# Kernel tuning notes

Hardware: AMD Instinct MI355X
Metric: run time of the kernel (lower is better)

## Reference

```python
import jax, jax.numpy as jnp
import numpy as np

N = 50000        # nodes
E = 800000       # edges
R = 8            # relations
G = 64           # g_dim
H1 = 64          # h1_dim
H2 = 32          # h2_dim (per-head for transformer, output for sage)
HEADS = 4
EPS = 1e-5       # BatchNorm eps


def setup_inputs() -> dict:
    key = jax.random.key(0)
    ks = jax.random.split(key, 16)
    def rn(k, shape, scale=0.05):
        return jax.random.normal(k, shape, dtype=jnp.float32) * scale
    return {
        "node_features": jax.random.normal(ks[0], (N, G), dtype=jnp.float32),
        "node_type": jax.random.randint(ks[1], (N,), 0, 3),
        "edge_index": jax.random.randint(ks[2], (2, E), 0, N),
        "edge_type": jax.random.randint(ks[3], (E,), 0, R),
        # RGCNConv params (per-relation weight + root weight + bias)
        "rgcn_w": rn(ks[4], (R, G, H1)),
        "rgcn_root": rn(ks[5], (G, H1)),
        "rgcn_bias": jnp.zeros((H1,), jnp.float32),
        "bn1_g": jnp.ones((H1,), jnp.float32),
        "bn1_b": jnp.zeros((H1,), jnp.float32),
        # TransformerConv params (q/k/v projections + skip)
        "wq": rn(ks[6], (H1, HEADS * H2)), "bq": jnp.zeros((HEADS * H2,), jnp.float32),
        "wk": rn(ks[7], (H1, HEADS * H2)), "bk": jnp.zeros((HEADS * H2,), jnp.float32),
        "wv": rn(ks[8], (H1, HEADS * H2)), "bv": jnp.zeros((HEADS * H2,), jnp.float32),
        "wskip": rn(ks[9], (H1, HEADS * H2)), "bskip": jnp.zeros((HEADS * H2,), jnp.float32),
        "bn2_g": jnp.ones((HEADS * H2,), jnp.float32),
        "bn2_b": jnp.zeros((HEADS * H2,), jnp.float32),
        # SAGEConv params (lin_l on aggregated neighbors has bias; lin_r on root has none)
        "sage_wl": rn(ks[10], (HEADS * H2, H2)), "sage_bl": jnp.zeros((H2,), jnp.float32),
        "sage_wr": rn(ks[11], (HEADS * H2, H2)),
        "bn3_g": jnp.ones((H2,), jnp.float32),
        "bn3_b": jnp.zeros((H2,), jnp.float32),
    }


def _bn(x, g, b):
    # BatchNorm1d in training mode: biased batch statistics over nodes
    m = x.mean(0)
    v = x.var(0)
    return g * (x - m) * jax.lax.rsqrt(v + EPS) + b


def _match(res, d):
    # F.pad(res, (0, d - c)): pads with zeros if d > c, truncates if d < c
    c = res.shape[1]
    if d > c:
        return jnp.pad(res, ((0, 0), (0, d - c)))
    return res[:, :d]


def _forward(node_features, rgcn_w, rgcn_root, rgcn_bias, bn1_g, bn1_b,
             wq, bq, wk, bk, wv, bv, wskip, bskip, bn2_g, bn2_b,
             sage_wl, sage_bl, sage_wr, bn3_g, bn3_b,
             edge_index, edge_type):
    src, dst = edge_index[0], edge_index[1]
    x = node_features
    residual = x

    # ---- RGCNConv: per-relation transform, per-relation mean aggregation, sum over relations ----
    xr = jnp.einsum('nf,rfh->nrh', x, rgcn_w)            # [N,R,H1]
    msg = xr[src, edge_type]                              # [E,H1]
    seg = dst * R + edge_type                             # segment per (node, relation)
    sums = jax.ops.segment_sum(msg, seg, num_segments=N * R)
    cnt = jax.ops.segment_sum(jnp.ones((E,), msg.dtype), seg, num_segments=N * R)
    agg = (sums / jnp.maximum(cnt, 1.0)[:, None]).reshape(N, R, H1).sum(1)
    h = agg + x @ rgcn_root + rgcn_bias
    h = jax.nn.leaky_relu(_bn(h, bn1_g, bn1_b))
    x = h + _match(residual, h.shape[1])
    residual = x

    # ---- TransformerConv: edge softmax attention, concat heads, + skip projection ----
    q = (x @ wq + bq).reshape(N, HEADS, H2)
    k = (x @ wk + bk).reshape(N, HEADS, H2)
    v = (x @ wv + bv).reshape(N, HEADS, H2)
    logits = (q[dst] * k[src]).sum(-1) / jnp.sqrt(jnp.float32(H2))  # [E,HEADS]
    mx = jax.ops.segment_max(logits, dst, num_segments=N)
    ex = jnp.exp(logits - mx[dst])
    den = jax.ops.segment_sum(ex, dst, num_segments=N)
    alpha = ex / jnp.maximum(den[dst], 1e-16)
    out = jax.ops.segment_sum(alpha[:, :, None] * v[src], dst, num_segments=N)
    h = out.reshape(N, HEADS * H2) + x @ wskip + bskip
    h = jax.nn.leaky_relu(_bn(h, bn2_g, bn2_b))
    x = h + _match(residual, h.shape[1])
    residual = x

    # ---- SAGEConv: mean neighbor aggregation + root transform ----
    nsum = jax.ops.segment_sum(x[src], dst, num_segments=N)
    ncnt = jax.ops.segment_sum(jnp.ones((E,), x.dtype), dst, num_segments=N)
    nmean = nsum / jnp.maximum(ncnt, 1.0)[:, None]
    h = nmean @ sage_wl + sage_bl + x @ sage_wr
    h = jax.nn.leaky_relu(_bn(h, bn3_g, bn3_b))
    return h + _match(residual, h.shape[1])


def reference(node_features, node_type, edge_index, edge_type,
              rgcn_w, rgcn_root, rgcn_bias, bn1_g, bn1_b,
              wq, bq, wk, bk, wv, bv, wskip, bskip, bn2_g, bn2_b,
              sage_wl, sage_bl, sage_wr, bn3_g, bn3_b):
    # node_type is unused by the original forward
    return _forward(node_features, rgcn_w, rgcn_root, rgcn_bias, bn1_g, bn1_b,
                    wq, bq, wk, bk, wv, bv, wskip, bskip, bn2_g, bn2_b,
                    sage_wl, sage_bl, sage_wr, bn3_g, bn3_b,
                    edge_index, edge_type)
```

## Files before the change

kernel.cpp:

```cpp
#include <hip/hip_runtime.h>
#include <stdint.h>

#define NN 50000
#define NE 800000
#define NR (NN*8)
#define SCAN_BS 512
#define NB2 782
#define INV_N (1.0f/50000.0f)
#define BN_EPS 1e-5f

typedef unsigned short ushort_t;
typedef unsigned char uchar_t;
typedef short bf16x8 __attribute__((ext_vector_type(8)));
typedef float f32x4 __attribute__((ext_vector_type(4)));
typedef float f32x2 __attribute__((ext_vector_type(2)));

__device__ __forceinline__ ushort_t f2bf(float f){
    unsigned int u = __float_as_uint(f);
    u += 0x7FFFu + ((u >> 16) & 1u);
    return (ushort_t)(u >> 16);
}
__device__ __forceinline__ float bf2f(ushort_t h){ return __uint_as_float(((unsigned int)h) << 16); }
__device__ __forceinline__ float bflo(unsigned int u){ return __uint_as_float(u << 16); }
__device__ __forceinline__ float bfhi(unsigned int u){ return __uint_as_float(u & 0xFFFF0000u); }

__device__ __forceinline__ unsigned int f4_to_fp8(float a, float b, float c, float d){
    int v = __builtin_amdgcn_cvt_pk_fp8_f32(a, b, 0, false);
    v = __builtin_amdgcn_cvt_pk_fp8_f32(c, d, v, true);
    return (unsigned int)v;
}
__device__ __forceinline__ void fp8_to_f4(unsigned int u, float& a, float& b, float& c, float& d){
    f32x2 lo = __builtin_amdgcn_cvt_pk_f32_fp8(u, false);
    f32x2 hi = __builtin_amdgcn_cvt_pk_f32_fp8(u, true);
    a = lo.x; b = lo.y; c = hi.x; d = hi.y;
}

__global__ void k_deg(const int* __restrict__ ei, const int* __restrict__ et,
                      int* __restrict__ deg, uint2* __restrict__ sr){
    int e = blockIdx.x*256 + threadIdx.x;
    if (e < NE){
        int seg = ei[NE + e]*8 + et[e];
        int rank = atomicAdd(&deg[seg], 1);
        uint2 o; o.x = (unsigned)seg; o.y = (unsigned)rank;
        sr[e] = o;
    }
}

__global__ void k_scan1(const int* __restrict__ deg, int* __restrict__ tmp, int* __restrict__ bsum){
    __shared__ int s[SCAN_BS];
    int t = threadIdx.x;
    int i = blockIdx.x*SCAN_BS + t;
    s[t] = (i < NR) ? deg[i] : 0;
    __syncthreads();
    for (int off = 1; off < SCAN_BS; off <<= 1){
        int add = (t >= off) ? s[t-off] : 0;
        __syncthreads();
        s[t] += add;
        __syncthreads();
    }
    if (i < NR) tmp[i] = s[t];
    if (t == SCAN_BS-1) bsum[blockIdx.x] = s[t];
}

__global__ void k_scan2(int* __restrict__ bsum){
    __shared__ int s[NB2];
    int t = threadIdx.x;
    if (t < NB2) s[t] = bsum[t];
    __syncthreads();
    if (t == 0){
        int acc = 0;
        for (int i = 0; i < NB2; ++i){ acc += s[i]; s[i] = acc; }
    }
    __syncthreads();
    if (t < NB2) bsum[t] = s[t];
}

__global__ void k_scan3(const int* __restrict__ tmp, const int* __restrict__ bsum, int* __restrict__ rs){
    int i = blockIdx.x*256 + threadIdx.x;
    if (i < NR){
        int b = i >> 9;
        int off = (b > 0) ? bsum[b-1] : 0;
        rs[i+1] = tmp[i] + off;
        if (i == 0) rs[0] = 0;
    }
}

__global__ void k_fill(const int* __restrict__ ei, const uint2* __restrict__ sr,
                       const int* __restrict__ rs, int* __restrict__ csr){
    int e = blockIdx.x*256 + threadIdx.x;
    if (e < NE){
        uint2 s = sr[e];
        csr[rs[s.x] + (int)s.y] = ei[e];
    }
}

__global__ void k_prep(const float* __restrict__ nf,
                       const float* __restrict__ rgcn_w, const float* __restrict__ root,
                       const float* __restrict__ wq, const float* __restrict__ wk,
                       const float* __restrict__ wv, const float* __restrict__ wsk,
                       const float* __restrict__ bq, const float* __restrict__ bk,
                       const float* __restrict__ bv, const float* __restrict__ bsk,
                       const float* __restrict__ wl, const float* __restrict__ wr,
                       ushort_t* __restrict__ xb, uchar_t* __restrict__ xb8,
                       ushort_t* __restrict__ Wcat,
                       ushort_t* __restrict__ Wt2, float* __restrict__ bcat,
                       ushort_t* __restrict__ Wsage){
    int i = blockIdx.x*256 + threadIdx.x;
    const int NXB = NN*16;
    if (i < NXB){
        float4 v = ((const float4*)nf)[i];
        ushort4 h;
        h.x = f2bf(v.x); h.y = f2bf(v.y); h.z = f2bf(v.z); h.w = f2bf(v.w);
        ((ushort4*)xb)[i] = h;
        ((unsigned int*)xb8)[i] = f4_to_fp8(v.x, v.y, v.z, v.w);
        return;
    }
    int j = i - NXB;
    if (j < 64*576){
        int h = j / 576, k = j - h*576;
        float v = (k < 512) ? rgcn_w[(size_t)k*64 + h] : root[(size_t)(k-512)*64 + h];
        Wcat[j] = f2bf(v);
    } else if (j < 64*576 + 512*64){
        int jj = j - 64*576;
        int c = jj >> 6, k = jj & 63;
        int mt = c >> 7, cc = c & 127;
        const float* W = (mt==0)?wq:(mt==1)?wk:(mt==2)?wv:wsk;
        Wt2[jj] = f2bf(W[(size_t)k*128 + cc]);
    } else if (j < 64*576 + 512*64 + 512){
        int c = j - (64*576 + 512*64);
        int mt = c >> 7, cc = c & 127;
        const float* B = (mt==0)?bq:(mt==1)?bk:(mt==2)?bv:bsk;
        bcat[c] = B[cc];
    } else if (j < 64*576 + 512*64 + 512 + 32*256){
        int jj = j - (64*576 + 512*64 + 512);
        int c = jj >> 8, k = jj & 255;
        float v = (k < 128) ? wr[(size_t)k*32 + c] : wl[(size_t)(k-128)*32 + c];
        Wsage[jj] = f2bf(v);
    }
}

__global__ __launch_bounds__(256) void rgcn_fused(const ushort_t* __restrict__ xb,
                                                  const uchar_t* __restrict__ xb8,
                                                  const int* __restrict__ rs,
                                                  const int* __restrict__ csr,
                                                  const ushort_t* __restrict__ Wcat,
                                                  const float* __restrict__ bias,
                                                  float* __restrict__ h1pre){
    __shared__ ushort_t Ml[16*520];
    int w = threadIdx.x >> 6, lane = threadIdx.x & 63;
    int quad = lane >> 4, l4 = lane & 15;
    int row0 = blockIdx.x * 16;
    int n0 = row0 + w*4;
    int rsel = (lane < 9 ? lane : 8);
    int rb = rs[n0*8 + rsel];
    int eb0 = __shfl(rb, 0);
    int dg0 = __shfl(rb, 8) - eb0;
    int idx = (lane < dg0) ? csr[eb0 + lane] : 0;
    for (int j = 0; j < 4; ++j){
        int lrow = (w*4 + j)*520;
        int ebase = __shfl(rb, 0);
        int enext = __shfl(rb, 8);
        int rb_next = 0, idxn = 0;
        if (j < 3){
            rb_next = rs[(n0 + j + 1)*8 + rsel];
            idxn = csr[min(enext + lane, NE - 1)];
        }
        int e0a = __shfl(rb, quad),     e1a = __shfl(rb, quad + 1);
        int e0b = __shfl(rb, quad + 4), e1b = __shfl(rb, quad + 5);
        int oa = e0a - ebase, la = e1a - e0a;
        int ob = e0b - ebase, lb = e1b - e0b;
        int ml = max(la, lb);
        ml = max(ml, __shfl_xor(ml, 16));
        ml = max(ml, __shfl_xor(ml, 32));
        float aa0=0.f, aa1=0.f, aa2=0.f, aa3=0.f;
        float ab0=0.f, ab1=0.f, ab2=0.f, ab3=0.f;
        for (int i = 0; i < ml; i += 4){
            int sA[4], sB[4];
            bool vA[4], vB[4];
#pragma unroll
            for (int u = 0; u < 4; ++u){
                int jA = oa + i + u, jB = ob + i + u;
                vA[u] = (i + u) < la;
                vB[u] = (i + u) < lb;
                int tA = __shfl(idx, jA & 63);
                int tB = __shfl(idx, jB & 63);
                if (jA >= 64 && vA[u]) tA = csr[ebase + jA];
                if (jB >= 64 && vB[u]) tB = csr[ebase + jB];
                sA[u] = vA[u] ? tA : 0;
                sB[u] = vB[u] ? tB : 0;
            }
            unsigned int uA[4], uB[4];
#pragma unroll
            for (int u = 0; u < 4; ++u){
                uA[u] = *(const unsigned int*)(xb8 + (size_t)sA[u]*64 + l4*4);
                uB[u] = *(const unsigned int*)(xb8 + (size_t)sB[u]*64 + l4*4);
            }
#pragma unroll
            for (int u = 0; u < 4; ++u){
                float f0,f1,f2,f3;
                fp8_to_f4(uA[u],f0,f1,f2,f3);
                if (vA[u]){ aa0+=f0; aa1+=f1; aa2+=f2; aa3+=f3; }
                fp8_to_f4(uB[u],f0,f1,f2,f3);
                if (vB[u]){ ab0+=f0; ab1+=f1; ab2+=f2; ab3+=f3; }
            }
        }
        float inva = 1.f / fmaxf((float)la, 1.f);
        float invb = 1.f / fmaxf((float)lb, 1.f);
        ushort4 oA, oB;
        oA.x = f2bf(aa0*inva); oA.y = f2bf(aa1*inva); oA.z = f2bf(aa2*inva); oA.w = f2bf(aa3*inva);
        oB.x = f2bf(ab0*invb); oB.y = f2bf(ab1*invb); oB.z = f2bf(ab2*invb); oB.w = f2bf(ab3*invb);
        *(ushort4*)&Ml[lrow + quad*64 + l4*4] = oA;
        *(ushort4*)&Ml[lrow + (quad + 4)*64 + l4*4] = oB;
        if (j < 3){
            rb = rb_next;
            int ebn = __shfl(rb, 0);
            int dgn = __shfl(rb, 8) - ebn;
            idx = (lane < dgn) ? idxn : 0;
        }
    }
    __syncthreads();
    int m = l4;
    f32x4 acc = {};
#pragma unroll
    for (int kt = 0; kt < 18; ++kt){
        int kk = kt*32 + quad*8;
        bf16x8 a;
        if (kt < 16) a = *(const bf16x8*)&Ml[m*520 + kk];
        else         a = *(const bf16x8*)(xb + (size_t)(row0 + m)*64 + (kk - 512));
        bf16x8 b = *(const bf16x8*)(Wcat + (size_t)(w*16 + m)*576 + kk);
        acc = __builtin_amdgcn_mfma_f32_16x16x32_bf16(a, b, acc, 0, 0, 0);
    }
    int col = w*16 + m;
    float bz = bias[col];
#pragma unroll
    for (int i = 0; i < 4; ++i){
        int rr = row0 + quad*4 + i;
        h1pre[(size_t)rr*64 + col] = acc[i] + bz;
    }
}

__global__ void bn1_finalize(const float* __restrict__ sums, const float* __restrict__ sumsq,
                             const float* __restrict__ g1, const float* __restrict__ b1,
                             float* __restrict__ A1, float* __restrict__ C1){
    int c = threadIdx.x;
    if (c < 64){
        float m = sums[c] * INV_N;
        float v = sumsq[c] * INV_N - m*m;
        float rsv = rsqrtf(fmaxf(v, 0.f) + BN_EPS);
        float A = rsv * g1[c];
        A1[c] = A;
        C1[c] = b1[c] - m * A;
    }
}

#define QS 132
#define BS 68
__global__ __launch_bounds__(256) void gemm_qkvs(const float* __restrict__ h1pre,
                                                 const float* __restrict__ nf,
                                                 const float* __restrict__ A1, const float* __restrict__ C1,
                                                 const ushort_t* __restrict__ Wt2,
                                                 const float* __restrict__ bcat,
                                                 ushort_t* __restrict__ qb,
                                                 uchar_t* __restrict__ kb8,
                                                 ushort_t* __restrict__ vb,
                                                 ushort_t* __restrict__ sb){
    __shared__ ushort_t Bs[256*BS];
    __shared__ ushort_t pl[4][16*QS];
    int w = threadIdx.x >> 6, lane = threadIdx.x & 63;
    int m = lane & 15, quad = lane >> 4;
    int r0 = blockIdx.x*64 + w*16;
    int cg = blockIdx.y;
    int row = r0 + m;
    {
        int t = threadIdx.x;
        const ushort_t* wsrc = Wt2 + (size_t)cg*256*64;
#pragma unroll
        for (int u0 = 0; u0 < 8; ++u0){
            int u = u0*256 + t;
            int r = u >> 3, c8 = (u & 7)*8;
            *(uint4*)&Bs[r*BS + c8] = *(const uint4*)(wsrc + u*8);
        }
    }
    bf16x8 afrag[2];
#pragma unroll
    for (int kt = 0; kt < 2; ++kt){
        int db = kt*32 + quad*8;
        bf16x8 f = (bf16x8){0,0,0,0,0,0,0,0};
        if (row < NN){
            float4 h0 = *(const float4*)(h1pre + (size_t)row*64 + db);
            float4 h1 = *(const float4*)(h1pre + (size_t)row*64 + db + 4);
            float4 n0 = *(const float4*)(nf + (size_t)row*64 + db);
            float4 n1 = *(const float4*)(nf + (size_t)row*64 + db + 4);
            float4 a0 = *(const float4*)(A1 + db);
            float4 a1 = *(const float4*)(A1 + db + 4);
            float4 c0 = *(const float4*)(C1 + db);
            float4 c1 = *(const float4*)(C1 + db + 4);
            float hh[8] = {h0.x,h0.y,h0.z,h0.w,h1.x,h1.y,h1.z,h1.w};
            float nn[8] = {n0.x,n0.y,n0.z,n0.w,n1.x,n1.y,n1.z,n1.w};
            float AA[8] = {a0.x,a0.y,a0.z,a0.w,a1.x,a1.y,a1.z,a1.w};
            float CC[8] = {c0.x,c0.y,c0.z,c0.w,c1.x,c1.y,c1.z,c1.w};
#pragma unroll
            for (int e = 0; e < 8; ++e){
                float y = fmaf(hh[e], AA[e], CC[e]);
                y = (y >= 0.f) ? y : 0.01f*y;
                f[e] = (short)f2bf(y + nn[e]);
            }
        }
        afrag[kt] = f;
    }
    __syncthreads();
    f32x4 acc[16] = {};
#pragma unroll
    for (int kt = 0; kt < 2; ++kt){
        int kk = kt*32 + quad*8;
#pragma unroll
        for (int ct = 0; ct < 16; ++ct){
            bf16x8 b = *(const bf16x8*)&Bs[(size_t)(ct*16 + m)*BS + kk];
            acc[ct] = __builtin_amdgcn_mfma_f32_16x16x32_bf16(afrag[kt], b, acc[ct], 0, 0, 0);
        }
    }
#pragma unroll
    for (int ct = 0; ct < 8; ++ct){
        int g = cg*256 + ct*16 + m;
        float bz = bcat[g];
        int cc = g & 127;
#pragma unroll
        for (int i = 0; i < 4; ++i)
            pl[w][(quad*4 + i)*QS + cc] = f2bf(acc[ct][i] + bz);
    }
    if (cg == 0){
#pragma unroll
        for (int t = 0; t < 4; ++t){
            int u = t*64 + lane;
            int r = u >> 4, c = (u & 15)*8;
            int gr = r0 + r;
            if (gr < NN) *(uint4*)(qb + (size_t)gr*128 + c) = *(const uint4*)&pl[w][r*QS + c];
        }
    } else {
#pragma unroll
        for (int t = 0; t < 4; ++t){
            int u = t*64 + lane;
            int r = u >> 4, c = (u & 15)*8;
            int gr = r0 + r;
            if (gr < NN) *(uint4*)(vb + (size_t)gr*128 + c) = *(const uint4*)&pl[w][r*QS + c];
        }
    }
#pragma unroll
    for (int ct = 8; ct < 16; ++ct){
        int g = cg*256 + ct*16 + m;
        float bz = bcat[g];
        int cc = g & 127;
#pragma unroll
        for (int i = 0; i < 4; ++i)
            pl[w][(quad*4 + i)*QS + cc] = f2bf(acc[ct][i] + bz);
    }
    if (cg == 0){
#pragma unroll
        for (int t = 0; t < 4; ++t){
            int u = t*64 + lane;
            int r = u >> 4, c = (u & 15)*8;
            int gr = r0 + r;
            if (gr < NN){
                uint4 kk4 = *(const uint4*)&pl[w][r*QS + c];
                uint2 o;
                o.x = f4_to_fp8(bflo(kk4.x), bfhi(kk4.x), bflo(kk4.y), bfhi(kk4.y));
                o.y = f4_to_fp8(bflo(kk4.z), bfhi(kk4.z), bflo(kk4.w), bfhi(kk4.w));
                *(uint2*)(kb8 + (size_t)gr*128 + c) = o;
            }
        }
    } else {
#pragma unroll
        for (int t = 0; t < 4; ++t){
            int u = t*64 + lane;
            int r = u >> 4, c = (u & 15)*8;
            int gr = r0 + r;
            if (gr < NN) *(uint4*)(sb + (size_t)gr*128 + c) = *(const uint4*)&pl[w][r*QS + c];
        }
    }
}

__global__ __launch_bounds__(256) void sage_gemm(const ushort_t* __restrict__ x2b,
                                                 const ushort_t* __restrict__ nmeanb,
                                                 const ushort_t* __restrict__ Wsage,
                                                 const float* __restrict__ bl,
                                                 float* __restrict__ h3){
    int wv = threadIdx.x >> 6, lane = threadIdx.x & 63;
    int r0 = blockIdx.x*64 + wv*16;
    int m = lane & 15, quad = lane >> 4;
    int row = r0 + m;
    f32x4 acc[2] = {};
#pragma unroll
    for (int kt = 0; kt < 8; ++kt){
        int kk = kt*32 + quad*8;
        bf16x8 a;
        if (row < NN){
            const ushort_t* ap = (kt < 4) ? (x2b + (size_t)row*128 + kk)
                                          : (nmeanb + (size_t)row*128 + (kk - 128));
            a = *(const bf16x8*)ap;
        } else {
            a = (bf16x8){0,0,0,0,0,0,0,0};
        }
#pragma unroll
        for (int ct = 0; ct < 2; ++ct){
            bf16x8 b = *(const bf16x8*)(Wsage + (size_t)(ct*16 + m)*256 + kk);
            acc[ct] = __builtin_amdgcn_mfma_f32_16x16x32_bf16(a, b, acc[ct], 0, 0, 0);
        }
    }
#pragma unroll
    for (int ct = 0; ct < 2; ++ct){
        int col = ct*16 + m;
        float bz = bl[col];
#pragma unroll
        for (int i = 0; i < 4; ++i){
            int rr = r0 + quad*4 + i;
            if (rr < NN) h3[(size_t)rr*32 + col] = acc[ct][i] + bz;
        }
    }
}

template<int C>
__global__ __launch_bounds__(256) void bn_stats(const float* __restrict__ X, int ld,
                                                float* __restrict__ sums, float* __restrict__ sumsq){
    __shared__ float s1[256], s2[256];
    int t = threadIdx.x;
    int c = t & (C-1);
    const int rpb = 256 / C;
    int r = blockIdx.x * rpb + (t / C);
    int rstride = gridDim.x * rpb;
    float a = 0.f, b = 0.f;
    for (; r < NN; r += rstride){
        float v = X[(size_t)r*ld + c];
        a += v; b += v*v;
    }
    s1[t] = a; s2[t] = b;
    __syncthreads();
    for (int off = 128; off >= C; off >>= 1){
        if (t < off){ s1[t] += s1[t+off]; s2[t] += s2[t+off]; }
        __syncthreads();
    }
    if (t < C){ atomicAdd(&sums[t], s1[t]); atomicAdd(&sumsq[t], s2[t]); }
}

__device__ __forceinline__ float bn_leaky(float z, float m, float rsv, float g, float b){
    float y = (z - m) * rsv * g + b;
    return y >= 0.f ? y : 0.01f * y;
}

__global__ void bn_apply2(const float* __restrict__ h2, const float* __restrict__ h1pre,
                          const float* __restrict__ nf,
                          const float* __restrict__ g1, const float* __restrict__ b1,
                          const float* __restrict__ s1, const float* __restrict__ q1,
                          const float* __restrict__ g2, const float* __restrict__ b2,
                          const float* __restrict__ s2, const float* __restrict__ q2,
                          float* __restrict__ x2r, ushort_t* __restrict__ x2b,
                          uchar_t* __restrict__ x28){
    int i = blockIdx.x*256 + threadIdx.x;
    if (i >= NN*128) return;
    int n = i >> 7, c = i & 127;
    float m2 = s2[c] * INV_N;
    float v2 = q2[c] * INV_N - m2*m2;
    float rsv2 = rsqrtf(fmaxf(v2, 0.f) + BN_EPS);
    float val = bn_leaky(h2[i], m2, rsv2, g2[c], b2[c]);
    if (c < 64){
        float m1 = s1[c] * INV_N;
        float v1 = q1[c] * INV_N - m1*m1;
        float rsv1 = rsqrtf(fmaxf(v1, 0.f) + BN_EPS);
        val += bn_leaky(h1pre[(size_t)n*64 + c], m1, rsv1, g1[c], b1[c]) + nf[(size_t)n*64 + c];
    }
    if (c < 32) x2r[(size_t)n*32 + c] = val;
    x2b[i] = f2bf(val);
    int p = __builtin_amdgcn_cvt_pk_fp8_f32(val, val, 0, false);
    x28[i] = (uchar_t)(p & 0xFF);
}

__global__ void bn_apply3(const float* __restrict__ h3, const float* __restrict__ x2r,
                          const float* __restrict__ g, const float* __restrict__ b,
                          const float* __restrict__ sums, const float* __restrict__ sumsq,
                          float* __restrict__ out){
    int i = blockIdx.x*256 + threadIdx.x;
    if (i >= NN*32) return;
    int c = i & 31;
    float m = sums[c] * INV_N;
    float v = sumsq[c] * INV_N - m*m;
    float rsv = rsqrtf(fmaxf(v, 0.f) + BN_EPS);
    out[i] = bn_leaky(h3[i], m, rsv, g[c], b[c]) + x2r[i];
}

__global__ __launch_bounds__(256) void attn_kernel(const ushort_t* __restrict__ qb,
                                                   const uchar_t* __restrict__ kb8,
                                                   const ushort_t* __restrict__ vb,
                                                   const ushort_t* __restrict__ sb,
                                                   const int* __restrict__ rs,
                                                   const int* __restrict__ csr,
                                                   float* __restrict__ h2){
    int w = threadIdx.x >> 6, lane = threadIdx.x & 63;
    int n = blockIdx.x*4 + w;
    if (n >= NN) return;
    int half = lane >> 5, l5 = lane & 31;
    int e0 = rs[n*8], e1 = rs[n*8 + 8];
    int deg = e1 - e0;
    uint2 qu = *(const uint2*)(qb + (size_t)n*128 + l5*4);
    uint2 sbv = *(const uint2*)(sb + (size_t)n*128 + l5*4);
    float q0 = bflo(qu.x), q1 = bfhi(qu.x), q2 = bflo(qu.y), q3 = bfhi(qu.y);
    const float scale = 0.17677669529663687f;
    int idx = 0;
    if (lane < deg) idx = csr[e0 + lane];
    int dcap = min(deg, 64);
    int nt = (dcap + 7) >> 3;
    float den = 0.f, a0 = 0.f, a1 = 0.f, a2 = 0.f, a3 = 0.f;
    for (int t = 0; t < nt; ++t){
        int i2 = t*8 + half*4;
        int j0 = i2, j1 = i2+1, j2 = i2+2, j3 = i2+3;
        bool v0 = j0 < dcap, v1 = j1 < dcap, v2 = j2 < dcap, v3 = j3 < dcap;
        int s0 = __shfl(idx, j0 & 63); s0 = v0 ? s0 : 0;
        int s1 = __shfl(idx, j1 & 63); s1 = v1 ? s1 : 0;
        int s2 = __shfl(idx, j2 & 63); s2 = v2 ? s2 : 0;
        int s3 = __shfl(idx, j3 & 63); s3 = v3 ? s3 : 0;
        unsigned int ku0 = *(const unsigned int*)(kb8 + (size_t)s0*128 + l5*4);
        unsigned int ku1 = *(const unsigned int*)(kb8 + (size_t)s1*128 + l5*4);
        unsigned int ku2 = *(const unsigned int*)(kb8 + (size_t)s2*128 + l5*4);
        unsigned int ku3 = *(const unsigned int*)(kb8 + (size_t)s3*128 + l5*4);
        uint2 vv0 = *(const uint2*)(vb + (size_t)s0*128 + l5*4);
        uint2 vv1 = *(const uint2*)(vb + (size_t)s1*128 + l5*4);
        uint2 vv2 = *(const uint2*)(vb + (size_t)s2*128 + l5*4);
        uint2 vv3 = *(const uint2*)(vb + (size_t)s3*128 + l5*4);
        float ka, kb_, kc, kd;
        fp8_to_f4(ku0, ka, kb_, kc, kd);
        float p0 = q0*ka + q1*kb_ + q2*kc + q3*kd;
        fp8_to_f4(ku1, ka, kb_, kc, kd);
        float p1 = q0*ka + q1*kb_ + q2*kc + q3*kd;
        fp8_to_f4(ku2, ka, kb_, kc, kd);
        float p2 = q0*ka + q1*kb_ + q2*kc + q3*kd;
        fp8_to_f4(ku3, ka, kb_, kc, kd);
        float p3 = q0*ka + q1*kb_ + q2*kc + q3*kd;
        p0 += __shfl_xor(p0, 1); p1 += __shfl_xor(p1, 1); p2 += __shfl_xor(p2, 1); p3 += __shfl_xor(p3, 1);
        p0 += __shfl_xor(p0, 2); p1 += __shfl_xor(p1, 2); p2 += __shfl_xor(p2, 2); p3 += __shfl_xor(p3, 2);
        p0 += __shfl_xor(p0, 4); p1 += __shfl_xor(p1, 4); p2 += __shfl_xor(p2, 4); p3 += __shfl_xor(p3, 4);
        float w0 = v0 ? __expf(p0 * scale) : 0.f;
        float w1 = v1 ? __expf(p1 * scale) : 0.f;
        float w2 = v2 ? __expf(p2 * scale) : 0.f;
        float w3 = v3 ? __expf(p3 * scale) : 0.f;
        den += w0 + w1 + w2 + w3;
        a0 += w0*bflo(vv0.x) + w1*bflo(vv1.x) + w2*bflo(vv2.x) + w3*bflo(vv3.x);
        a1 += w0*bfhi(vv0.x) + w1*bfhi(vv1.x) + w2*bfhi(vv2.x) + w3*bfhi(vv3.x);
        a2 += w0*bflo(vv0.y) + w1*bflo(vv1.y) + w2*bflo(vv2.y) + w3*bflo(vv3.y);
        a3 += w0*bfhi(vv0.y) + w1*bfhi(vv1.y) + w2*bfhi(vv2.y) + w3*bfhi(vv3.y);
    }
    for (int e = 64 + half; e < deg; e += 2){
        int s = csr[e0 + e];
        unsigned int ku = *(const unsigned int*)(kb8 + (size_t)s*128 + l5*4);
        uint2 vv = *(const uint2*)(vb + (size_t)s*128 + l5*4);
        float ka, kb_, kc, kd;
        fp8_to_f4(ku, ka, kb_, kc, kd);
        float p = q0*ka + q1*kb_ + q2*kc + q3*kd;
        p += __shfl_xor(p, 1);
        p += __shfl_xor(p, 2);
        p += __shfl_xor(p, 4);
        float wg = __expf(p * scale);
        den += wg;
        a0 += wg*bflo(vv.x); a1 += wg*bfhi(vv.x);
        a2 += wg*bflo(vv.y); a3 += wg*bfhi(vv.y);
    }
    den += __shfl_xor(den, 32);
    a0 += __shfl_xor(a0, 32); a1 += __shfl_xor(a1, 32);
    a2 += __shfl_xor(a2, 32); a3 += __shfl_xor(a3, 32);
    if (half == 0){
        float inv = (den > 0.f) ? 1.f/den : 0.f;
        float4 o;
        o.x = bflo(sbv.x) + a0*inv;
        o.y = bfhi(sbv.x) + a1*inv;
        o.z = bflo(sbv.y) + a2*inv;
        o.w = bfhi(sbv.y) + a3*inv;
        *(float4*)(h2 + (size_t)n*128 + l5*4) = o;
    }
}

__global__ __launch_bounds__(256) void sage_agg(const uchar_t* __restrict__ x28,
                                                const int* __restrict__ rs,
                                                const int* __restrict__ csr,
                                                ushort_t* __restrict__ nmeanb){
    int w = threadIdx.x >> 6, lane = threadIdx.x & 63;
    int n = blockIdx.x*4 + w;
    if (n >= NN) return;
    int half = lane >> 5, l5 = lane & 31;
    int e0 = rs[n*8], e1 = rs[n*8 + 8];
    int deg = e1 - e0;
    int idx = 0;
    if (lane < deg) idx = csr[e0 + lane];
    int dcap = min(deg, 64);
    int nt = (dcap + 7) >> 3;
    float a0 = 0.f, a1 = 0.f, a2 = 0.f, a3 = 0.f;
    for (int t = 0; t < nt; ++t){
        int i2 = t*8 + half*4;
        int j0 = i2, j1 = i2+1, j2 = i2+2, j3 = i2+3;
        bool v0 = j0 < dcap, v1 = j1 < dcap, v2 = j2 < dcap, v3 = j3 < dcap;
        int s0 = __shfl(idx, j0 & 63); s0 = v0 ? s0 : 0;
        int s1 = __shfl(idx, j1 & 63); s1 = v1 ? s1 : 0;
        int s2 = __shfl(idx, j2 & 63); s2 = v2 ? s2 : 0;
        int s3 = __shfl(idx, j3 & 63); s3 = v3 ? s3 : 0;
        unsigned int u0 = *(const unsigned int*)(x28 + (size_t)s0*128 + l5*4);
        unsigned int u1 = *(const unsigned int*)(x28 + (size_t)s1*128 + l5*4);
        unsigned int u2 = *(const unsigned int*)(x28 + (size_t)s2*128 + l5*4);
        unsigned int u3 = *(const unsigned int*)(x28 + (size_t)s3*128 + l5*4);
        float fa, fb, fc, fd;
        if (v0){ fp8_to_f4(u0, fa, fb, fc, fd); a0 += fa; a1 += fb; a2 += fc; a3 += fd; }
        if (v1){ fp8_to_f4(u1, fa, fb, fc, fd); a0 += fa; a1 += fb; a2 += fc; a3 += fd; }
        if (v2){ fp8_to_f4(u2, fa, fb, fc, fd); a0 += fa; a1 += fb; a2 += fc; a3 += fd; }
        if (v3){ fp8_to_f4(u3, fa, fb, fc, fd); a0 += fa; a1 += fb; a2 += fc; a3 += fd; }
    }
    for (int e = 64 + half; e < deg; e += 2){
        int s = csr[e0 + e];
        unsigned int u = *(const unsigned int*)(x28 + (size_t)s*128 + l5*4);
        float fa, fb, fc, fd;
        fp8_to_f4(u, fa, fb, fc, fd);
        a0 += fa; a1 += fb; a2 += fc; a3 += fd;
    }
    a0 += __shfl_xor(a0, 32); a1 += __shfl_xor(a1, 32);
    a2 += __shfl_xor(a2, 32); a3 += __shfl_xor(a3, 32);
    if (half == 0){
        float inv = 1.f / fmaxf((float)deg, 1.f);
        ushort4 o;
        o.x = f2bf(a0*inv); o.y = f2bf(a1*inv); o.z = f2bf(a2*inv); o.w = f2bf(a3*inv);
        *(ushort4*)(nmeanb + (size_t)n*128 + l5*4) = o;
    }
}

extern "C" void kernel_launch(void* const* d_in, const int* in_sizes, int n_in,
                              void* d_out, int out_size, void* d_ws, size_t ws_size,
                              hipStream_t stream){
    const float* nf      = (const float*)d_in[0];
    const int*   ei      = (const int*)d_in[2];
    const int*   et      = (const int*)d_in[3];
    const float* rgcn_w  = (const float*)d_in[4];
    const float* root    = (const float*)d_in[5];
    const float* rbias   = (const float*)d_in[6];
    const float* bn1g    = (const float*)d_in[7];
    const float* bn1b    = (const float*)d_in[8];
    const float* wq      = (const float*)d_in[9];
    const float* bq      = (const float*)d_in[10];
    const float* wk      = (const float*)d_in[11];
    const float* bk      = (const float*)d_in[12];
    const float* wv      = (const float*)d_in[13];
    const float* bv      = (const float*)d_in[14];
    const float* wsk     = (const float*)d_in[15];
    const float* bsk     = (const float*)d_in[16];
    const float* bn2g    = (const float*)d_in[17];
    const float* bn2b    = (const float*)d_in[18];
    const float* wl      = (const float*)d_in[19];
    const float* bl      = (const float*)d_in[20];
    const float* wr      = (const float*)d_in[21];
    const float* bn3g    = (const float*)d_in[22];
    const float* bn3b    = (const float*)d_in[23];
    float* out = (float*)d_out;

    char* base = (char*)d_ws;
    size_t off = 0;
    auto take = [&](size_t bytes) -> char* {
        char* p = base + off;
        off += (bytes + 255) & ~(size_t)255;
        return p;
    };
    int*      deg    = (int*)take((size_t)NR*4);
    float*    bns    = (float*)take(1024*4);
    char*     zend   = base + off;
    int*      rs     = (int*)take((size_t)(NR+1)*4);
    int*      tmp    = (int*)take((size_t)NR*4);
    int*      bsum   = (int*)take(1024*4);
    uint2*    sr     = (uint2*)take((size_t)NE*8);
    int*      csr    = (int*)take((size_t)NE*4);
    ushort_t* Wcat   = (ushort_t*)take(64*576*2);
    ushort_t* Wt2    = (ushort_t*)take(512*64*2);
    float*    bcat   = (float*)take(512*4);
    ushort_t* Wsage  = (ushort_t*)take(32*256*2);
    ushort_t* xb     = (ushort_t*)take((size_t)NN*64*2);
    uchar_t*  xb8    = (uchar_t*)take((size_t)NN*64);
    float*    h1pre  = (float*)take((size_t)NN*64*4);
    float*    h2     = (float*)take((size_t)NN*128*4);
    float*    x2r    = (float*)take((size_t)NN*32*4);
    ushort_t* sb     = (ushort_t*)take((size_t)NN*128*2);
    char*     bigA   = take((size_t)NN*512*2);
    if (off > ws_size) return;

    ushort_t* qb     = (ushort_t*)(bigA + (size_t)NN*128);
    ushort_t* vb     = (ushort_t*)(bigA + (size_t)NN*384);
    uchar_t*  kb8    = (uchar_t*)(bigA + (size_t)NN*640);
    ushort_t* x2b    = (ushort_t*)bigA;
    uchar_t*  x28    = (uchar_t*)(bigA + (size_t)NN*256);
    ushort_t* nmeanb = (ushort_t*)(bigA + (size_t)NN*512);
    float*    h3     = (float*)(bigA + (size_t)NN*768);

    hipMemsetAsync(deg, 0, (size_t)(zend - (char*)deg), stream);

    const int PREP_N = NN*16 + 64*576 + 512*64 + 512 + 32*256;
    k_prep <<<(PREP_N+255)/256, 256, 0, stream>>>(nf, rgcn_w, root, wq, wk, wv, wsk,
                                                  bq, bk, bv, bsk, wl, wr,
                                                  xb, xb8, Wcat, Wt2, bcat, Wsage);
    k_deg  <<<(NE+255)/256, 256, 0, stream>>>(ei, et, deg, sr);
    k_scan1<<<NB2, SCAN_BS, 0, stream>>>(deg, tmp, bsum);
    k_scan2<<<1, 1024, 0, stream>>>(bsum);
    k_scan3<<<(NR+255)/256, 256, 0, stream>>>(tmp, bsum, rs);
    k_fill <<<(NE+255)/256, 256, 0, stream>>>(ei, sr, rs, csr);

    const int NB4 = (NN + 3) / 4;
    const int NBG = (NN + 63) / 64;

    rgcn_fused<<<NN/16, 256, 0, stream>>>(xb, xb8, rs, csr, Wcat, rbias, h1pre);
    bn_stats<64><<<256, 256, 0, stream>>>(h1pre, 64, bns + 0, bns + 64);
    bn1_finalize<<<1, 64, 0, stream>>>(bns + 0, bns + 64, bn1g, bn1b, bns + 448, bns + 512);

    gemm_qkvs<<<dim3(NBG, 2), 256, 0, stream>>>(h1pre, nf, bns + 448, bns + 512,
                                                Wt2, bcat, qb, kb8, vb, sb);
    attn_kernel<<<NB4, 256, 0, stream>>>(qb, kb8, vb, sb, rs, csr, h2);
    bn_stats<128><<<256, 256, 0, stream>>>(h2, 128, bns + 128, bns + 256);
    bn_apply2<<<(NN*128+255)/256, 256, 0, stream>>>(h2, h1pre, nf,
                                                    bn1g, bn1b, bns + 0, bns + 64,
                                                    bn2g, bn2b, bns + 128, bns + 256,
                                                    x2r, x2b, x28);

    sage_agg<<<NB4, 256, 0, stream>>>(x28, rs, csr, nmeanb);
    sage_gemm<<<NBG, 256, 0, stream>>>(x2b, nmeanb, Wsage, bl, h3);
    bn_stats<32><<<256, 256, 0, stream>>>(h3, 32, bns + 384, bns + 416);
    bn_apply3<<<(NN*32+255)/256, 256, 0, stream>>>(h3, x2r, bn3g, bn3b, bns + 384, bns + 416, out);
}
```

Measured before the change: 410.5 us.

## Aggregate RGCN per node with LDS atomics and store V as fp8

The CSR now stores each neighbour's relation in the low 3 bits of the source index, and a per-edge weight of 1/degree is precomputed at fill time. The RGCN kernel walks each node's full edge list once and accumulates weighted neighbour features into fp32 shared memory with atomic adds, replacing the per-relation segmented walk. Separately, the V projection is stored as fp8 instead of bf16, halving the bytes the attention kernel gathers per edge. The cost is shared-memory atomics, an extra weight array read, and lower precision in V.

```diff
diff --git a/kernel.cpp b/kernel.cpp
--- a/kernel.cpp
+++ b/kernel.cpp
@@ -8,6 +8,7 @@
 #define NB2 782
 #define INV_N (1.0f/50000.0f)
 #define BN_EPS 1e-5f
+#define ROWF 532
 
 typedef unsigned short ushort_t;
 typedef unsigned char uchar_t;
@@ -86,11 +87,16 @@
 }
 
 __global__ void k_fill(const int* __restrict__ ei, const uint2* __restrict__ sr,
-                       const int* __restrict__ rs, int* __restrict__ csr){
+                       const int* __restrict__ rs, int* __restrict__ csr,
+                       float* __restrict__ wgt){
     int e = blockIdx.x*256 + threadIdx.x;
     if (e < NE){
         uint2 s = sr[e];
-        csr[rs[s.x] + (int)s.y] = ei[e];
+        int b = rs[s.x];
+        int dgs = rs[s.x + 1] - b;
+        int pos = b + (int)s.y;
+        csr[pos] = ei[e]*8 + (int)(s.x & 7u);
+        wgt[pos] = 1.f / (float)dgs;
     }
 }
 
@@ -139,99 +145,93 @@
     }
 }
 
-__global__ __launch_bounds__(256) void rgcn_fused(const ushort_t* __restrict__ xb,
-                                                  const uchar_t* __restrict__ xb8,
-                                                  const int* __restrict__ rs,
-                                                  const int* __restrict__ csr,
-                                                  const ushort_t* __restrict__ Wcat,
-                                                  const float* __restrict__ bias,
-                                                  float* __restrict__ h1pre){
-    __shared__ ushort_t Ml[16*520];
+__global__ __launch_bounds__(256) void rgcn_fused2(const ushort_t* __restrict__ xb,
+                                                   const uchar_t* __restrict__ xb8,
+                                                   const int* __restrict__ rs,
+                                                   const int* __restrict__ csr,
+                                                   const float* __restrict__ wgt,
+                                                   const ushort_t* __restrict__ Wcat,
+                                                   const float* __restrict__ rbias,
+                                                   float* __restrict__ h1pre){
+    __shared__ float M[16*ROWF];
     int w = threadIdx.x >> 6, lane = threadIdx.x & 63;
-    int quad = lane >> 4, l4 = lane & 15;
+    int grp = lane >> 4, l4 = lane & 15;
     int row0 = blockIdx.x * 16;
-    int n0 = row0 + w*4;
-    int rsel = (lane < 9 ? lane : 8);
-    int rb = rs[n0*8 + rsel];
-    int eb0 = __shfl(rb, 0);
-    int dg0 = __shfl(rb, 8) - eb0;
-    int idx = (lane < dg0) ? csr[eb0 + lane] : 0;
+    {
+        float4 z = {0.f,0.f,0.f,0.f};
+        const int nf4 = 16*ROWF/4;
+        for (int i = threadIdx.x; i < nf4; i += 256) ((float4*)M)[i] = z;
+    }
+    __syncthreads();
     for (int j = 0; j < 4; ++j){
-        int lrow = (w*4 + j)*520;
-        int ebase = __shfl(rb, 0);
-        int enext = __shfl(rb, 8);
-        int rb_next = 0, idxn = 0;
-        if (j < 3){
-            rb_next = rs[(n0 + j + 1)*8 + rsel];
-            idxn = csr[min(enext + lane, NE - 1)];
-        }
-        int e0a = __shfl(rb, quad),     e1a = __shfl(rb, quad + 1);
-        int e0b = __shfl(rb, quad + 4), e1b = __shfl(rb, quad + 5);
-        int oa = e0a - ebase, la = e1a - e0a;
-        int ob = e0b - ebase, lb = e1b - e0b;
-        int ml = max(la, lb);
-        ml = max(ml, __shfl_xor(ml, 16));
-        ml = max(ml, __shfl_xor(ml, 32));
-        float aa0=0.f, aa1=0.f, aa2=0.f, aa3=0.f;
-        float ab0=0.f, ab1=0.f, ab2=0.f, ab3=0.f;
-        for (int i = 0; i < ml; i += 4){
-            int sA[4], sB[4];
-            bool vA[4], vB[4];
+        int n = row0 + w*4 + j;
+        int e0 = rs[n*8], e1 = rs[n*8 + 8];
+        int deg = e1 - e0;
+        int idx = 0; float wle = 0.f;
+        if (lane < deg){ idx = csr[e0 + lane]; wle = wgt[e0 + lane]; }
+        int dcap = min(deg, 64);
+        float* Mrow = M + (w*4 + j)*ROWF;
+        for (int t = 0; t < dcap; t += 16){
+            int sj[4]; float wj[4];
 #pragma unroll
             for (int u = 0; u < 4; ++u){
-                int jA = oa + i + u, jB = ob + i + u;
-                vA[u] = (i + u) < la;
-                vB[u] = (i + u) < lb;
-                int tA = __shfl(idx, jA & 63);
-                int tB = __shfl(idx, jB & 63);
-                if (jA >= 64 && vA[u]) tA = csr[ebase + jA];
-                if (jB >= 64 && vB[u]) tB = csr[ebase + jB];
-                sA[u] = vA[u] ? tA : 0;
-                sB[u] = vB[u] ? tB : 0;
+                int jj = t + grp*4 + u;
+                bool v = jj < dcap;
+                int s = __shfl(idx, jj & 63);
+                float ww = __shfl(wle, jj & 63);
+                sj[u] = v ? s : 0;
+                wj[u] = v ? ww : 0.f;
             }
-            unsigned int uA[4], uB[4];
-#pragma unroll
-            for (int u = 0; u < 4; ++u){
-                uA[u] = *(const unsigned int*)(xb8 + (size_t)sA[u]*64 + l4*4);
-                uB[u] = *(const unsigned int*)(xb8 + (size_t)sB[u]*64 + l4*4);
-            }
+            unsigned int ux[4];
+#pragma unroll
+            for (int u = 0; u < 4; ++u)
+                ux[u] = *(const unsigned int*)(xb8 + ((size_t)(unsigned)(sj[u] >> 3) << 6) + l4*4);
 #pragma unroll
             for (int u = 0; u < 4; ++u){
                 float f0,f1,f2,f3;
-                fp8_to_f4(uA[u],f0,f1,f2,f3);
-                if (vA[u]){ aa0+=f0; aa1+=f1; aa2+=f2; aa3+=f3; }
-                fp8_to_f4(uB[u],f0,f1,f2,f3);
-                if (vB[u]){ ab0+=f0; ab1+=f1; ab2+=f2; ab3+=f3; }
+                fp8_to_f4(ux[u], f0, f1, f2, f3);
+                float* p = Mrow + (sj[u] & 7)*64 + l4*4;
+                atomicAdd(p+0, wj[u]*f0);
+                atomicAdd(p+1, wj[u]*f1);
+                atomicAdd(p+2, wj[u]*f2);
+                atomicAdd(p+3, wj[u]*f3);
             }
         }
-        float inva = 1.f / fmaxf((float)la, 1.f);
-        float invb = 1.f / fmaxf((float)lb, 1.f);
-        ushort4 oA, oB;
-        oA.x = f2bf(aa0*inva); oA.y = f2bf(aa1*inva); oA.z = f2bf(aa2*inva); oA.w = f2bf(aa3*inva);
-        oB.x = f2bf(ab0*invb); oB.y = f2bf(ab1*invb); oB.z = f2bf(ab2*invb); oB.w = f2bf(ab3*invb);
-        *(ushort4*)&Ml[lrow + quad*64 + l4*4] = oA;
-        *(ushort4*)&Ml[lrow + (quad + 4)*64 + l4*4] = oB;
-        if (j < 3){
-            rb = rb_next;
-            int ebn = __shfl(rb, 0);
-            int dgn = __shfl(rb, 8) - ebn;
-            idx = (lane < dgn) ? idxn : 0;
+        for (int e = 64 + grp; e < deg; e += 4){
+            int s = csr[e0 + e];
+            float ww = wgt[e0 + e];
+            unsigned int ux = *(const unsigned int*)(xb8 + ((size_t)(unsigned)(s >> 3) << 6) + l4*4);
+            float f0,f1,f2,f3;
+            fp8_to_f4(ux, f0, f1, f2, f3);
+            float* p = Mrow + (s & 7)*64 + l4*4;
+            atomicAdd(p+0, ww*f0);
+            atomicAdd(p+1, ww*f1);
+            atomicAdd(p+2, ww*f2);
+            atomicAdd(p+3, ww*f3);
         }
     }
     __syncthreads();
-    int m = l4;
+    int m = l4, quad = grp;
     f32x4 acc = {};
 #pragma unroll
     for (int kt = 0; kt < 18; ++kt){
         int kk = kt*32 + quad*8;
         bf16x8 a;
-        if (kt < 16) a = *(const bf16x8*)&Ml[m*520 + kk];
-        else         a = *(const bf16x8*)(xb + (size_t)(row0 + m)*64 + (kk - 512));
+        if (kt < 16){
+            float4 v0 = *(const float4*)(M + m*ROWF + kk);
+            float4 v1 = *(const float4*)(M + m*ROWF + kk + 4);
+            a[0] = (short)f2bf(v0.x); a[1] = (short)f2bf(v0.y);
+            a[2] = (short)f2bf(v0.z); a[3] = (short)f2bf(v0.w);
+            a[4] = (short)f2bf(v1.x); a[5] = (short)f2bf(v1.y);
+            a[6] = (short)f2bf(v1.z); a[7] = (short)f2bf(v1.w);
+        } else {
+            a = *(const bf16x8*)(xb + (size_t)(row0 + m)*64 + (kk - 512));
+        }
         bf16x8 b = *(const bf16x8*)(Wcat + (size_t)(w*16 + m)*576 + kk);
         acc = __builtin_amdgcn_mfma_f32_16x16x32_bf16(a, b, acc, 0, 0, 0);
     }
     int col = w*16 + m;
-    float bz = bias[col];
+    float bz = rbias[col];
 #pragma unroll
     for (int i = 0; i < 4; ++i){
         int rr = row0 + quad*4 + i;
@@ -262,7 +262,7 @@
                                                  const float* __restrict__ bcat,
                                                  ushort_t* __restrict__ qb,
                                                  uchar_t* __restrict__ kb8,
-                                                 ushort_t* __restrict__ vb,
+                                                 uchar_t* __restrict__ vb8,
                                                  ushort_t* __restrict__ sb){
     __shared__ ushort_t Bs[256*BS];
     __shared__ ushort_t pl[4][16*QS];
@@ -342,7 +342,13 @@
             int u = t*64 + lane;
             int r = u >> 4, c = (u & 15)*8;
             int gr = r0 + r;
-            if (gr < NN) *(uint4*)(vb + (size_t)gr*128 + c) = *(const uint4*)&pl[w][r*QS + c];
+            if (gr < NN){
+                uint4 vv4 = *(const uint4*)&pl[w][r*QS + c];
+                uint2 o;
+                o.x = f4_to_fp8(bflo(vv4.x), bfhi(vv4.x), bflo(vv4.y), bfhi(vv4.y));
+                o.y = f4_to_fp8(bflo(vv4.z), bfhi(vv4.z), bflo(vv4.w), bfhi(vv4.w));
+                *(uint2*)(vb8 + (size_t)gr*128 + c) = o;
+            }
         }
     }
 #pragma unroll
@@ -488,7 +494,7 @@
 
 __global__ __launch_bounds__(256) void attn_kernel(const ushort_t* __restrict__ qb,
                                                    const uchar_t* __restrict__ kb8,
-                                                   const ushort_t* __restrict__ vb,
+                                                   const uchar_t* __restrict__ vb8,
                                                    const ushort_t* __restrict__ sb,
                                                    const int* __restrict__ rs,
                                                    const int* __restrict__ csr,
@@ -512,18 +518,18 @@
         int i2 = t*8 + half*4;
         int j0 = i2, j1 = i2+1, j2 = i2+2, j3 = i2+3;
         bool v0 = j0 < dcap, v1 = j1 < dcap, v2 = j2 < dcap, v3 = j3 < dcap;
-        int s0 = __shfl(idx, j0 & 63); s0 = v0 ? s0 : 0;
-        int s1 = __shfl(idx, j1 & 63); s1 = v1 ? s1 : 0;
-        int s2 = __shfl(idx, j2 & 63); s2 = v2 ? s2 : 0;
-        int s3 = __shfl(idx, j3 & 63); s3 = v3 ? s3 : 0;
+        int s0 = __shfl(idx, j0 & 63); s0 = v0 ? (s0 >> 3) : 0;
+        int s1 = __shfl(idx, j1 & 63); s1 = v1 ? (s1 >> 3) : 0;
+        int s2 = __shfl(idx, j2 & 63); s2 = v2 ? (s2 >> 3) : 0;
+        int s3 = __shfl(idx, j3 & 63); s3 = v3 ? (s3 >> 3) : 0;
         unsigned int ku0 = *(const unsigned int*)(kb8 + (size_t)s0*128 + l5*4);
         unsigned int ku1 = *(const unsigned int*)(kb8 + (size_t)s1*128 + l5*4);
         unsigned int ku2 = *(const unsigned int*)(kb8 + (size_t)s2*128 + l5*4);
         unsigned int ku3 = *(const unsigned int*)(kb8 + (size_t)s3*128 + l5*4);
-        uint2 vv0 = *(const uint2*)(vb + (size_t)s0*128 + l5*4);
-        uint2 vv1 = *(const uint2*)(vb + (size_t)s1*128 + l5*4);
-        uint2 vv2 = *(const uint2*)(vb + (size_t)s2*128 + l5*4);
-        uint2 vv3 = *(const uint2*)(vb + (size_t)s3*128 + l5*4);
+        unsigned int vu0 = *(const unsigned int*)(vb8 + (size_t)s0*128 + l5*4);
+        unsigned int vu1 = *(const unsigned int*)(vb8 + (size_t)s1*128 + l5*4);
+        unsigned int vu2 = *(const unsigned int*)(vb8 + (size_t)s2*128 + l5*4);
+        unsigned int vu3 = *(const unsigned int*)(vb8 + (size_t)s3*128 + l5*4);
         float ka, kb_, kc, kd;
         fp8_to_f4(ku0, ka, kb_, kc, kd);
         float p0 = q0*ka + q1*kb_ + q2*kc + q3*kd;
@@ -541,15 +547,20 @@
         float w2 = v2 ? __expf(p2 * scale) : 0.f;
         float w3 = v3 ? __expf(p3 * scale) : 0.f;
         den += w0 + w1 + w2 + w3;
-        a0 += w0*bflo(vv0.x) + w1*bflo(vv1.x) + w2*bflo(vv2.x) + w3*bflo(vv3.x);
-        a1 += w0*bfhi(vv0.x) + w1*bfhi(vv1.x) + w2*bfhi(vv2.x) + w3*bfhi(vv3.x);
-        a2 += w0*bflo(vv0.y) + w1*bflo(vv1.y) + w2*bflo(vv2.y) + w3*bflo(vv3.y);
-        a3 += w0*bfhi(vv0.y) + w1*bfhi(vv1.y) + w2*bfhi(vv2.y) + w3*bfhi(vv3.y);
+        float va, vb_, vc, vd;
+        fp8_to_f4(vu0, va, vb_, vc, vd);
+        a0 = fmaf(w0, va, a0); a1 = fmaf(w0, vb_, a1); a2 = fmaf(w0, vc, a2); a3 = fmaf(w0, vd, a3);
+        fp8_to_f4(vu1, va, vb_, vc, vd);
+        a0 = fmaf(w1, va, a0); a1 = fmaf(w1, vb_, a1); a2 = fmaf(w1, vc, a2); a3 = fmaf(w1, vd, a3);
+        fp8_to_f4(vu2, va, vb_, vc, vd);
+        a0 = fmaf(w2, va, a0); a1 = fmaf(w2, vb_, a1); a2 = fmaf(w2, vc, a2); a3 = fmaf(w2, vd, a3);
+        fp8_to_f4(vu3, va, vb_, vc, vd);
+        a0 = fmaf(w3, va, a0); a1 = fmaf(w3, vb_, a1); a2 = fmaf(w3, vc, a2); a3 = fmaf(w3, vd, a3);
     }
     for (int e = 64 + half; e < deg; e += 2){
-        int s = csr[e0 + e];
+        int s = csr[e0 + e] >> 3;
         unsigned int ku = *(const unsigned int*)(kb8 + (size_t)s*128 + l5*4);
-        uint2 vv = *(const uint2*)(vb + (size_t)s*128 + l5*4);
+        unsigned int vu = *(const unsigned int*)(vb8 + (size_t)s*128 + l5*4);
         float ka, kb_, kc, kd;
         fp8_to_f4(ku, ka, kb_, kc, kd);
         float p = q0*ka + q1*kb_ + q2*kc + q3*kd;
@@ -558,8 +569,9 @@
         p += __shfl_xor(p, 4);
         float wg = __expf(p * scale);
         den += wg;
-        a0 += wg*bflo(vv.x); a1 += wg*bfhi(vv.x);
-        a2 += wg*bflo(vv.y); a3 += wg*bfhi(vv.y);
+        float va, vb_, vc, vd;
+        fp8_to_f4(vu, va, vb_, vc, vd);
+        a0 = fmaf(wg, va, a0); a1 = fmaf(wg, vb_, a1); a2 = fmaf(wg, vc, a2); a3 = fmaf(wg, vd, a3);
     }
     den += __shfl_xor(den, 32);
     a0 += __shfl_xor(a0, 32); a1 += __shfl_xor(a1, 32);
@@ -594,10 +606,10 @@
         int i2 = t*8 + half*4;
         int j0 = i2, j1 = i2+1, j2 = i2+2, j3 = i2+3;
         bool v0 = j0 < dcap, v1 = j1 < dcap, v2 = j2 < dcap, v3 = j3 < dcap;
-        int s0 = __shfl(idx, j0 & 63); s0 = v0 ? s0 : 0;
-        int s1 = __shfl(idx, j1 & 63); s1 = v1 ? s1 : 0;
-        int s2 = __shfl(idx, j2 & 63); s2 = v2 ? s2 : 0;
-        int s3 = __shfl(idx, j3 & 63); s3 = v3 ? s3 : 0;
+        int s0 = __shfl(idx, j0 & 63); s0 = v0 ? (s0 >> 3) : 0;
+        int s1 = __shfl(idx, j1 & 63); s1 = v1 ? (s1 >> 3) : 0;
+        int s2 = __shfl(idx, j2 & 63); s2 = v2 ? (s2 >> 3) : 0;
+        int s3 = __shfl(idx, j3 & 63); s3 = v3 ? (s3 >> 3) : 0;
         unsigned int u0 = *(const unsigned int*)(x28 + (size_t)s0*128 + l5*4);
         unsigned int u1 = *(const unsigned int*)(x28 + (size_t)s1*128 + l5*4);
         unsigned int u2 = *(const unsigned int*)(x28 + (size_t)s2*128 + l5*4);
@@ -609,7 +621,7 @@
         if (v3){ fp8_to_f4(u3, fa, fb, fc, fd); a0 += fa; a1 += fb; a2 += fc; a3 += fd; }
     }
     for (int e = 64 + half; e < deg; e += 2){
-        int s = csr[e0 + e];
+        int s = csr[e0 + e] >> 3;
         unsigned int u = *(const unsigned int*)(x28 + (size_t)s*128 + l5*4);
         float fa, fb, fc, fd;
         fp8_to_f4(u, fa, fb, fc, fd);
@@ -668,6 +680,7 @@
     int*      bsum   = (int*)take(1024*4);
     uint2*    sr     = (uint2*)take((size_t)NE*8);
     int*      csr    = (int*)take((size_t)NE*4);
+    float*    wgt    = (float*)take((size_t)NE*4);
     ushort_t* Wcat   = (ushort_t*)take(64*576*2);
     ushort_t* Wt2    = (ushort_t*)take(512*64*2);
     float*    bcat   = (float*)take(512*4);
@@ -682,7 +695,7 @@
     if (off > ws_size) return;
 
     ushort_t* qb     = (ushort_t*)(bigA + (size_t)NN*128);
-    ushort_t* vb     = (ushort_t*)(bigA + (size_t)NN*384);
+    uchar_t*  vb8    = (uchar_t*)(bigA + (size_t)NN*384);
     uchar_t*  kb8    = (uchar_t*)(bigA + (size_t)NN*640);
     ushort_t* x2b    = (ushort_t*)bigA;
     uchar_t*  x28    = (uchar_t*)(bigA + (size_t)NN*256);
@@ -699,18 +712,18 @@
     k_scan1<<<NB2, SCAN_BS, 0, stream>>>(deg, tmp, bsum);
     k_scan2<<<1, 1024, 0, stream>>>(bsum);
     k_scan3<<<(NR+255)/256, 256, 0, stream>>>(tmp, bsum, rs);
-    k_fill <<<(NE+255)/256, 256, 0, stream>>>(ei, sr, rs, csr);
+    k_fill <<<(NE+255)/256, 256, 0, stream>>>(ei, sr, rs, csr, wgt);
 
     const int NB4 = (NN + 3) / 4;
     const int NBG = (NN + 63) / 64;
 
-    rgcn_fused<<<NN/16, 256, 0, stream>>>(xb, xb8, rs, csr, Wcat, rbias, h1pre);
+    rgcn_fused2<<<NN/16, 256, 0, stream>>>(xb, xb8, rs, csr, wgt, Wcat, rbias, h1pre);
     bn_stats<64><<<256, 256, 0, stream>>>(h1pre, 64, bns + 0, bns + 64);
     bn1_finalize<<<1, 64, 0, stream>>>(bns + 0, bns + 64, bn1g, bn1b, bns + 448, bns + 512);
 
     gemm_qkvs<<<dim3(NBG, 2), 256, 0, stream>>>(h1pre, nf, bns + 448, bns + 512,
-                                                Wt2, bcat, qb, kb8, vb, sb);
-    attn_kernel<<<NB4, 256, 0, stream>>>(qb, kb8, vb, sb, rs, csr, h2);
+                                                Wt2, bcat, qb, kb8, vb8, sb);
+    attn_kernel<<<NB4, 256, 0, stream>>>(qb, kb8, vb8, sb, rs, csr, h2);
     bn_stats<128><<<256, 256, 0, stream>>>(h2, 128, bns + 128, bns + 256);
     bn_apply2<<<(NN*128+255)/256, 256, 0, stream>>>(h2, h1pre, nf,
                                                     bn1g, bn1b, bns + 0, bns + 64,
```

Result: slower. 767.8 us (+87.1%).
